# Performance work log

Measured on AMD Instinct MI355X. Metric: run time of the kernel, lower is better.

The kernel has to match this reference:

```python
import jax, jax.numpy as jnp
import numpy as np

EPS = float(np.finfo(np.float32).eps)
QMIN, QMAX = -128, 127


def setup_inputs() -> dict:
    key = jax.random.key(0)
    k_x, k_w, k_ws, k_b = jax.random.split(key, 4)
    M, K, N = 32768, 1024, 1024
    x = jax.random.normal(k_x, (M, K), dtype=jnp.float32)
    # per-channel symmetrically quantized, transposed weight: [K, N], values in [-128, 127]
    w_int8_t = jax.random.randint(k_w, (K, N), QMIN, QMAX + 1, dtype=jnp.int32).astype(jnp.int8)
    # per-out-channel scales (positive, float; torch uses float64, we use float32)
    w_scales = (jax.random.uniform(k_ws, (N,), dtype=jnp.float32) * 0.02 + 1e-4)
    # preprocessed column sums: w_int8_t.sum(dim=0)
    w_int8_t_sums = w_int8_t.astype(jnp.int32).sum(axis=0)
    bias = jax.random.normal(k_b, (N,), dtype=jnp.float32)
    return {
        "x": x,
        "w_int8_t": w_int8_t,
        "w_scales": w_scales,
        "w_int8_t_sums": w_int8_t_sums,
        "bias": bias,
    }


def reference(x, w_int8_t, w_scales, w_int8_t_sums, bias):
    # ---- dynamically_quantize_per_tensor (affine, int8) ----
    min_neg = jnp.minimum(jnp.min(x), jnp.float32(0.0))
    max_pos = jnp.maximum(jnp.max(x), jnp.float32(0.0))
    x_scale = jnp.maximum((max_pos - min_neg) / jnp.float32(QMAX - QMIN), EPS)
    x_zp = jnp.clip(QMIN - jnp.round(min_neg / x_scale), QMIN, QMAX)  # scalar
    x_q = jnp.clip(jnp.round(x / x_scale) + x_zp, QMIN, QMAX).astype(jnp.int8)

    # ---- int8 matmul with int32 accumulation (safe_int_mm equivalent) ----
    xw_i32 = jnp.matmul(
        x_q.astype(jnp.int32), w_int8_t.astype(jnp.int32)
    )  # [M, N] int32

    # ---- dequant with zero-point correction (quant_int8_matmul) ----
    mm_unscaled = xw_i32.astype(jnp.float32) - x_zp * w_int8_t_sums.astype(jnp.float32)
    y = x_scale * w_scales * mm_unscaled  # broadcast w_scales over N

    # ---- bias add (quant_int8_dynamic_linear) ----
    y = y + bias
    return y.astype(jnp.float32)
```

## Files before the change

kernel.cpp:

```cpp
#include <hip/hip_runtime.h>
#include <stdint.h>

#define M_DIM 32768
#define K_DIM 1024
#define N_DIM 1024

typedef int v4i __attribute__((ext_vector_type(4)));

__device__ __forceinline__ void gld_lds16(const void* g, void* lds) {
    __builtin_amdgcn_global_load_lds(
        (const __attribute__((address_space(1))) unsigned int*)g,
        (__attribute__((address_space(3))) unsigned int*)lds, 16, 0, 0);
}

__global__ void k_prep(const float* __restrict__ x,
                       float* __restrict__ pmin, float* __restrict__ pmax,
                       const int* __restrict__ w, int8_t* __restrict__ wt) {
    int t = threadIdx.x;
    if (blockIdx.x < 1024) {
        long gid = (long)blockIdx.x * 256 + t;
        const float4* x4 = (const float4*)x;
        const long n4 = (long)M_DIM * K_DIM / 4;
        float mn = INFINITY, mx = -INFINITY;
#pragma unroll 4
        for (long i = gid; i < n4; i += 1024 * 256) {
            float4 v = x4[i];
            mn = fminf(mn, fminf(fminf(v.x, v.y), fminf(v.z, v.w)));
            mx = fmaxf(mx, fmaxf(fmaxf(v.x, v.y), fmaxf(v.z, v.w)));
        }
        __shared__ float smn[256], smx[256];
        smn[t] = mn; smx[t] = mx;
        __syncthreads();
        for (int s = 128; s > 0; s >>= 1) {
            if (t < s) {
                smn[t] = fminf(smn[t], smn[t + s]);
                smx[t] = fmaxf(smx[t], smx[t + s]);
            }
            __syncthreads();
        }
        if (t == 0) { pmin[blockIdx.x] = smn[0]; pmax[blockIdx.x] = smx[0]; }
    } else {
        __shared__ int8_t tile[32][33];
        int b = blockIdx.x - 1024;
        int bn = (b & 31) * 32;
        int bk = (b >> 5) * 32;
        int tx = t & 31, ty = t >> 5;
#pragma unroll
        for (int i = 0; i < 32; i += 8)
            tile[ty + i][tx] = (int8_t)w[(long)(bk + ty + i) * N_DIM + bn + tx];
        __syncthreads();
#pragma unroll
        for (int i = 0; i < 32; i += 8)
            wt[(long)(bn + ty + i) * K_DIM + bk + tx] = tile[tx][ty + i];
    }
}

__global__ void k_finalize(const float* __restrict__ pmin,
                           const float* __restrict__ pmax,
                           float* __restrict__ sp) {
    int t = threadIdx.x;
    float mn = INFINITY, mx = -INFINITY;
    for (int i = t; i < 1024; i += 256) {
        mn = fminf(mn, pmin[i]);
        mx = fmaxf(mx, pmax[i]);
    }
    __shared__ float smn[256], smx[256];
    smn[t] = mn; smx[t] = mx;
    __syncthreads();
    for (int s = 128; s > 0; s >>= 1) {
        if (t < s) {
            smn[t] = fminf(smn[t], smn[t + s]);
            smx[t] = fmaxf(smx[t], smx[t + s]);
        }
        __syncthreads();
    }
    if (t == 0) {
        float min_neg = fminf(smn[0], 0.0f);
        float max_pos = fmaxf(smx[0], 0.0f);
        float scale = (max_pos - min_neg) / 255.0f;
        scale = fmaxf(scale, 1.1920928955078125e-07f);
        float zp = -128.0f - rintf(min_neg / scale);
        zp = fminf(fmaxf(zp, -128.0f), 127.0f);
        sp[0] = scale;
        sp[1] = zp;
    }
}

__device__ __forceinline__ unsigned q4(float4 v, float s, float zp) {
    int a = (int)fminf(fmaxf(rintf(v.x / s) + zp, -128.0f), 127.0f);
    int b = (int)fminf(fmaxf(rintf(v.y / s) + zp, -128.0f), 127.0f);
    int c = (int)fminf(fmaxf(rintf(v.z / s) + zp, -128.0f), 127.0f);
    int d = (int)fminf(fmaxf(rintf(v.w / s) + zp, -128.0f), 127.0f);
    return (a & 255) | ((b & 255) << 8) | ((c & 255) << 16) | ((d & 255) << 24);
}

__global__ void k_quant(const float* __restrict__ x,
                        const float* __restrict__ sp,
                        int8_t* __restrict__ xq) {
    float s = sp[0], zp = sp[1];
    const float4* x4 = (const float4*)x;
    unsigned* q4out = (unsigned*)xq;
    long base = (long)blockIdx.x * 1024;
    int t = threadIdx.x;
#pragma unroll
    for (int v = 0; v < 4; v++) {
        long i = base + (long)v * 256 + t;
        float4 val = x4[i];
        q4out[i] = q4(val, s, zp);
    }
}

__global__ __launch_bounds__(256) void k_gemm(
    const int8_t* __restrict__ xq, const int8_t* __restrict__ wt,
    const float* __restrict__ sp, const float* __restrict__ w_scales,
    const int* __restrict__ wsums, const float* __restrict__ bias,
    float* __restrict__ out) {
    __shared__ __align__(16) int8_t lds_a[2][128 * 64];
    __shared__ __align__(16) int8_t lds_b[2][128 * 64];

    const int t = threadIdx.x;
    const int orig = blockIdx.x;
    const int swz = (orig & 7) * 256 + (orig >> 3);
    const int m0 = (swz >> 3) * 128;
    const int n0 = (swz & 7) * 128;
    const int w = t >> 6, l = t & 63, quad = l >> 4, r = l & 15;
    const int wave_m = (w & 1) * 64, wave_n = (w >> 1) * 64;

    v4i acc[4][4];
#pragma unroll
    for (int i = 0; i < 4; i++)
#pragma unroll
        for (int j = 0; j < 4; j++) acc[i][j] = (v4i){0, 0, 0, 0};

    const int slot0 = t, slot1 = 256 + t;
    const int row0 = slot0 >> 2, s0 = slot0 & 3;
    const int row1 = slot1 >> 2, s1 = slot1 & 3;
    const int q0 = s0 ^ (row0 & 3) ^ ((row0 >> 2) & 3);
    const int q1 = s1 ^ (row1 & 3) ^ ((row1 >> 2) & 3);
    const int8_t* gA0 = xq + (long)(m0 + row0) * K_DIM + q0 * 16;
    const int8_t* gA1 = xq + (long)(m0 + row1) * K_DIM + q1 * 16;
    const int8_t* gB0 = wt + (long)(n0 + row0) * K_DIM + q0 * 16;
    const int8_t* gB1 = wt + (long)(n0 + row1) * K_DIM + q1 * 16;

#define STAGE(buf, kb)                                        \
    do {                                                      \
        gld_lds16(gA0 + (kb), lds_a[buf] + slot0 * 16);       \
        gld_lds16(gA1 + (kb), lds_a[buf] + slot1 * 16);       \
        gld_lds16(gB0 + (kb), lds_b[buf] + slot0 * 16);       \
        gld_lds16(gB1 + (kb), lds_b[buf] + slot1 * 16);       \
    } while (0)

    int ra[4], rb[4];
#pragma unroll
    for (int i = 0; i < 4; i++) {
        int mrow = wave_m + i * 16 + r;
        int sa = quad ^ (mrow & 3) ^ ((mrow >> 2) & 3);
        ra[i] = mrow * 64 + sa * 16;
        int nrow = wave_n + i * 16 + r;
        int sb = quad ^ (nrow & 3) ^ ((nrow >> 2) & 3);
        rb[i] = nrow * 64 + sb * 16;
    }

    STAGE(0, 0);
    __syncthreads();

    int cur = 0;
    for (int kb = 64; kb <= K_DIM; kb += 64) {
        if (kb < K_DIM) STAGE(cur ^ 1, kb);

        v4i af[4], bf[4];
#pragma unroll
        for (int i = 0; i < 4; i++) af[i] = *(const v4i*)(lds_a[cur] + ra[i]);
#pragma unroll
        for (int j = 0; j < 4; j++) bf[j] = *(const v4i*)(lds_b[cur] + rb[j]);
#pragma unroll
        for (int i = 0; i < 4; i++)
#pragma unroll
            for (int j = 0; j < 4; j++)
                acc[i][j] = __builtin_amdgcn_mfma_i32_16x16x64_i8(af[i], bf[j], acc[i][j], 0, 0, 0);

        __syncthreads();
        cur ^= 1;
    }
#undef STAGE

    const float scale = sp[0], zp = sp[1];
#pragma unroll
    for (int j = 0; j < 4; j++) {
        int n = n0 + wave_n + j * 16 + r;
        float sj = scale * w_scales[n];
        float cj = zp * (float)wsums[n];
        float bj = bias[n];
#pragma unroll
        for (int i = 0; i < 4; i++) {
            int mbase = m0 + wave_m + i * 16 + quad * 4;
#pragma unroll
            for (int e = 0; e < 4; e++) {
                out[(long)(mbase + e) * N_DIM + n] = sj * ((float)acc[i][j][e] - cj) + bj;
            }
        }
    }
}

extern "C" void kernel_launch(void* const* d_in, const int* in_sizes, int n_in,
                              void* d_out, int out_size, void* d_ws, size_t ws_size,
                              hipStream_t stream) {
    const float* x        = (const float*)d_in[0];
    const int*   w_int8_t = (const int*)d_in[1];
    const float* w_scales = (const float*)d_in[2];
    const int*   w_sums   = (const int*)d_in[3];
    const float* bias     = (const float*)d_in[4];
    float* out = (float*)d_out;

    float* wsf  = (float*)d_ws;
    float* pmin = wsf;
    float* pmax = wsf + 1024;
    float* sp   = wsf + 2048;
    int8_t* wt  = (int8_t*)d_ws + 16384;
    int8_t* xq  = (int8_t*)d_ws + 16384 + (size_t)K_DIM * N_DIM;

    k_prep<<<2048, 256, 0, stream>>>(x, pmin, pmax, w_int8_t, wt);
    k_finalize<<<1, 256, 0, stream>>>(pmin, pmax, sp);
    k_quant<<<8192, 256, 0, stream>>>(x, sp, xq);
    k_gemm<<<2048, 256, 0, stream>>>(xq, wt, sp, w_scales, w_sums, bias, out);
}
```

Before: 320.7 us.

## Fuse scale finalize into quant kernel and pipeline GEMM loads with explicit waitcnt

Drops the single-block finalize kernel: every quant block now redundantly reduces the 1024 partial min/max values itself and derives scale and zero-point, removing one launch and a serialization point. The GEMM main loop replaces __syncthreads with explicit vmcnt waits and raw barriers so the next tile's global-to-LDS loads stay in flight while the current tile computes, and raises wave priority around the MFMA block. This trades a small redundant reduction per quant block for the removed launch, and relies on hand-placed waitcnt and barrier ordering being correct for the async LDS loads.

```diff
diff --git a/kernel.cpp b/kernel.cpp
--- a/kernel.cpp
+++ b/kernel.cpp
@@ -55,37 +55,6 @@
     }
 }
 
-__global__ void k_finalize(const float* __restrict__ pmin,
-                           const float* __restrict__ pmax,
-                           float* __restrict__ sp) {
-    int t = threadIdx.x;
-    float mn = INFINITY, mx = -INFINITY;
-    for (int i = t; i < 1024; i += 256) {
-        mn = fminf(mn, pmin[i]);
-        mx = fmaxf(mx, pmax[i]);
-    }
-    __shared__ float smn[256], smx[256];
-    smn[t] = mn; smx[t] = mx;
-    __syncthreads();
-    for (int s = 128; s > 0; s >>= 1) {
-        if (t < s) {
-            smn[t] = fminf(smn[t], smn[t + s]);
-            smx[t] = fmaxf(smx[t], smx[t + s]);
-        }
-        __syncthreads();
-    }
-    if (t == 0) {
-        float min_neg = fminf(smn[0], 0.0f);
-        float max_pos = fmaxf(smx[0], 0.0f);
-        float scale = (max_pos - min_neg) / 255.0f;
-        scale = fmaxf(scale, 1.1920928955078125e-07f);
-        float zp = -128.0f - rintf(min_neg / scale);
-        zp = fminf(fmaxf(zp, -128.0f), 127.0f);
-        sp[0] = scale;
-        sp[1] = zp;
-    }
-}
-
 __device__ __forceinline__ unsigned q4(float4 v, float s, float zp) {
     int a = (int)fminf(fmaxf(rintf(v.x / s) + zp, -128.0f), 127.0f);
     int b = (int)fminf(fmaxf(rintf(v.y / s) + zp, -128.0f), 127.0f);
@@ -95,13 +64,38 @@
 }
 
 __global__ void k_quant(const float* __restrict__ x,
-                        const float* __restrict__ sp,
+                        const float* __restrict__ pmin,
+                        const float* __restrict__ pmax,
+                        float* __restrict__ sp,
                         int8_t* __restrict__ xq) {
-    float s = sp[0], zp = sp[1];
+    int t = threadIdx.x;
+    float mn = INFINITY, mx = -INFINITY;
+#pragma unroll
+    for (int i = 0; i < 4; i++) {
+        mn = fminf(mn, pmin[i * 256 + t]);
+        mx = fmaxf(mx, pmax[i * 256 + t]);
+    }
+    __shared__ float smn[256], smx[256];
+    smn[t] = mn; smx[t] = mx;
+    __syncthreads();
+    for (int ss = 128; ss > 0; ss >>= 1) {
+        if (t < ss) {
+            smn[t] = fminf(smn[t], smn[t + ss]);
+            smx[t] = fmaxf(smx[t], smx[t + ss]);
+        }
+        __syncthreads();
+    }
+    float min_neg = fminf(smn[0], 0.0f);
+    float max_pos = fmaxf(smx[0], 0.0f);
+    float s = (max_pos - min_neg) / 255.0f;
+    s = fmaxf(s, 1.1920928955078125e-07f);
+    float zp = -128.0f - rintf(min_neg / s);
+    zp = fminf(fmaxf(zp, -128.0f), 127.0f);
+    if (blockIdx.x == 0 && t == 0) { sp[0] = s; sp[1] = zp; }
+
     const float4* x4 = (const float4*)x;
     unsigned* q4out = (unsigned*)xq;
     long base = (long)blockIdx.x * 1024;
-    int t = threadIdx.x;
 #pragma unroll
     for (int v = 0; v < 4; v++) {
         long i = base + (long)v * 256 + t;
@@ -162,24 +156,34 @@
     }
 
     STAGE(0, 0);
-    __syncthreads();
 
     int cur = 0;
-    for (int kb = 64; kb <= K_DIM; kb += 64) {
-        if (kb < K_DIM) STAGE(cur ^ 1, kb);
+#pragma unroll 2
+    for (int kt = 0; kt < 16; ++kt) {
+        if (kt < 15) {
+            STAGE(cur ^ 1, (kt + 1) * 64);
+            asm volatile("s_waitcnt vmcnt(4)" ::: "memory");
+        } else {
+            asm volatile("s_waitcnt vmcnt(0)" ::: "memory");
+        }
+        asm volatile("s_barrier" ::: "memory");
 
         v4i af[4], bf[4];
 #pragma unroll
         for (int i = 0; i < 4; i++) af[i] = *(const v4i*)(lds_a[cur] + ra[i]);
 #pragma unroll
         for (int j = 0; j < 4; j++) bf[j] = *(const v4i*)(lds_b[cur] + rb[j]);
+
+        __builtin_amdgcn_s_setprio(1);
 #pragma unroll
         for (int i = 0; i < 4; i++)
 #pragma unroll
             for (int j = 0; j < 4; j++)
                 acc[i][j] = __builtin_amdgcn_mfma_i32_16x16x64_i8(af[i], bf[j], acc[i][j], 0, 0, 0);
-
-        __syncthreads();
+        __builtin_amdgcn_s_setprio(0);
+
+        if (kt < 15)
+            asm volatile("s_barrier" ::: "memory");
         cur ^= 1;
     }
 #undef STAGE
@@ -220,7 +224,6 @@
     int8_t* xq  = (int8_t*)d_ws + 16384 + (size_t)K_DIM * N_DIM;
 
     k_prep<<<2048, 256, 0, stream>>>(x, pmin, pmax, w_int8_t, wt);
-    k_finalize<<<1, 256, 0, stream>>>(pmin, pmax, sp);
-    k_quant<<<8192, 256, 0, stream>>>(x, sp, xq);
+    k_quant<<<8192, 256, 0, stream>>>(x, pmin, pmax, sp, xq);
     k_gemm<<<2048, 256, 0, stream>>>(xq, wt, sp, w_scales, w_sums, bias, out);
 }
```

Result: no change. 321.6 us (+0.3%).
